# Optimization experiments

Hardware: AMD Instinct MI355X
Metric: run time of the kernel (lower is better)

Reference implementation:

```python
import jax, jax.numpy as jnp
import numpy as np

B, S, NH, HD = 2, 2048, 32, 128     # batch seqs, tokens per seq, heads, head_dim
H = NH * HD                          # hidden = 4096
BLOCK = 64                           # paged KV-cache block size
NBLK = S // BLOCK                    # blocks per sequence
NUM_BLOCKS = B * NBLK                # total cache blocks


def alibi_slopes(n):
    # n is a power of two: slope_i = 2^(-8*(i+1)/n)
    return np.asarray([2.0 ** (-8.0 * (i + 1) / n) for i in range(n)], dtype=np.float32)


def setup_inputs() -> dict:
    key = jax.random.key(0)
    k1, k2, k3 = jax.random.split(key, 3)
    hidden_states = jax.random.normal(k1, (B * S, H), jnp.float32)
    w_pack = jax.random.normal(k2, (H, 3 * H), jnp.float32) * 0.02
    o_proj_w = jax.random.normal(k3, (H, H), jnp.float32) * 0.02
    k_cache = jnp.zeros((NUM_BLOCKS, BLOCK, NH, HD), jnp.float32)
    v_cache = jnp.zeros((NUM_BLOCKS, BLOCK, NH, HD), jnp.float32)
    block_offsets = jnp.arange(NUM_BLOCKS, dtype=jnp.int32).reshape(B, NBLK)
    return {
        "hidden_states": hidden_states,
        "w_pack": w_pack,
        "o_proj_w": o_proj_w,
        "k_cache": k_cache,
        "v_cache": v_cache,
        "block_offsets": block_offsets,
    }


def reference(hidden_states, w_pack, o_proj_w, k_cache, v_cache, block_offsets):
    # fused QKV projection, chunk(3, -1)
    qkv = hidden_states @ w_pack                      # [B*S, 3H]
    q, k, v = jnp.split(qkv, 3, axis=-1)
    q = q.reshape(B, S, NH, HD)
    k = k.reshape(B, NBLK, BLOCK, NH, HD)
    v = v.reshape(B, NBLK, BLOCK, NH, HD)

    # fill_kv_cache: scatter new K/V into paged cache blocks
    k_cache = k_cache.at[block_offsets].set(k)        # [NUM_BLOCKS, BLOCK, NH, HD]
    v_cache = v_cache.at[block_offsets].set(v)

    # paged read: gather non-contiguous blocks back per sequence
    kg = k_cache[block_offsets].reshape(B, S, NH, HD)
    vg = v_cache[block_offsets].reshape(B, S, NH, HD)

    slopes = jnp.asarray(alibi_slopes(NH))            # [NH]
    scale = 1.0 / jnp.sqrt(jnp.float32(HD))
    scores = jnp.einsum('bqhd,bkhd->bhqk', q, kg) * scale   # [B,NH,S,S]
    pos = jnp.arange(S)
    # ALiBi bias: slope * key_position (row-shift invariant under softmax)
    scores = scores + slopes[None, :, None, None] * pos[None, None, None, :]
    causal = pos[:, None] >= pos[None, :]             # [S,S]
    scores = jnp.where(causal[None, None], scores, jnp.float32(-1e30))
    probs = jax.nn.softmax(scores, axis=-1)
    attn = jnp.einsum('bhqk,bkhd->bqhd', probs, vg).reshape(B * S, H)
    return attn @ o_proj_w
```

## Files before the change

kernel.cpp:

```cpp
#include <hip/hip_runtime.h>
#include <hip/hip_bf16.h>
#include <stdint.h>

typedef __attribute__((ext_vector_type(4))) float f32x4;
typedef __attribute__((ext_vector_type(8))) __bf16 bf16x8;
typedef __attribute__((ext_vector_type(8))) unsigned short u16x8;
typedef __attribute__((ext_vector_type(4))) unsigned short u16x4;
typedef __attribute__((ext_vector_type(4))) unsigned int u32x4;

#define GLL16(g, l) __builtin_amdgcn_global_load_lds( \
    (const __attribute__((address_space(1))) unsigned int*)(uintptr_t)(g), \
    (__attribute__((address_space(3))) unsigned int*)(uintptr_t)(l), 16, 0, 0)

__device__ __forceinline__ unsigned short bf16u(float f) {
  return __builtin_bit_cast(unsigned short, __float2bfloat16(f));
}

#define PB 2
#define PS 2048
#define PNH 32
#define PHD 128
#define PH 4096
#define P3H 12288

__global__ __launch_bounds__(256)
void cvt_f32_bf16(const float* __restrict__ in, unsigned short* __restrict__ out, int n) {
  int stride = gridDim.x * blockDim.x;
  for (int i = blockIdx.x * blockDim.x + threadIdx.x; i * 8 < n; i += stride) {
    int base = i * 8;
    f32x4 a = *(const f32x4*)(in + base);
    f32x4 b = *(const f32x4*)(in + base + 4);
    u16x8 o;
#pragma unroll
    for (int j = 0; j < 4; ++j) { o[j] = bf16u(a[j]); o[4 + j] = bf16u(b[j]); }
    *(u16x8*)(out + base) = o;
  }
}

__global__ __launch_bounds__(256)
void transpose_cvt(const float* __restrict__ in, unsigned short* __restrict__ out,
                   int K, int N) {
  __shared__ __align__(16) unsigned short tile[64][68];
  int k0 = blockIdx.y * 64, n0 = blockIdx.x * 64;
  int t = threadIdx.x;
  int rr = t >> 4, cc = (t & 15) * 4;
#pragma unroll
  for (int p = 0; p < 4; ++p) {
    int r = rr + p * 16;
    f32x4 v = *(const f32x4*)(in + (size_t)(k0 + r) * N + n0 + cc);
    u16x4 w;
#pragma unroll
    for (int j = 0; j < 4; ++j) w[j] = bf16u(v[j]);
    *(u16x4*)&tile[r][cc] = w;
  }
  __syncthreads();
#pragma unroll
  for (int p = 0; p < 4; ++p) {
    int nl = rr + p * 16;
    u16x4 w;
#pragma unroll
    for (int j = 0; j < 4; ++j) w[j] = tile[cc + j][nl];
    *(u16x4*)(out + (size_t)(n0 + nl) * K + k0 + cc) = w;
  }
}

#define GLLP(TT, P) do { int sb_ = ((TT) & 3) << 15; \
    const unsigned short* s_ = (P) == 0 ? aSrc0 : (P) == 1 ? aSrc1 : (P) == 2 ? bSrc0 : bSrc1; \
    GLL16(s_ + (size_t)(TT) * 32, smem + sb_ + ((P) << 13) + (wave << 10)); } while (0)

#define RD_AV(DST, BUFP, I) DST[I] = *(const bf16x8*)((BUFP) + (((wm << 7) + ((I) << 4) + lr) << 6) + lchunk)
#define RD_BV(DST, BUFP, J) DST[J] = *(const bf16x8*)((BUFP) + 16384 + (((wn << 6) + ((J) << 4) + lr) << 6) + lchunk)

#define SGB __builtin_amdgcn_sched_group_barrier

#define TILE(TC, AC, AN, DOSTAGE, DOREAD, VM, DOBAR) do { \
    char* nA_ = smem + ((((TC) + 1) & 3) << 15); \
    __builtin_amdgcn_s_setprio(1); \
    _Pragma("unroll") \
    for (int g = 0; g < 4; ++g) { \
      if (DOREAD) { RD_AV(AN, nA_, 2 * g); RD_AV(AN, nA_, 2 * g + 1); } \
      if (DOSTAGE) GLLP((TC) + 3, g); \
      _Pragma("unroll") \
      for (int i = 2 * g; i < 2 * g + 2; ++i) \
        _Pragma("unroll") \
        for (int j = 0; j < 4; ++j) \
          acc[i][j] = __builtin_amdgcn_mfma_f32_16x16x32_bf16(AC[i], bvv[j], acc[i][j], 0, 0, 0); \
      SGB(0x100, 2, 0); SGB(0x020, 1, 0); SGB(0x008, 8, 0); \
    } \
    if (DOREAD) { RD_BV(bvv, nA_, 0); RD_BV(bvv, nA_, 1); RD_BV(bvv, nA_, 2); RD_BV(bvv, nA_, 3); } \
    __builtin_amdgcn_s_setprio(0); \
    if ((VM) == 4)      asm volatile("s_waitcnt vmcnt(4)" ::: "memory"); \
    else if ((VM) == 0) asm volatile("s_waitcnt vmcnt(0)" ::: "memory"); \
    if (DOBAR) __builtin_amdgcn_s_barrier(); \
  } while (0)

template<int OUTF32>
__global__ __launch_bounds__(512, 2)
void gemm256(const unsigned short* __restrict__ A, const unsigned short* __restrict__ Bt,
             void* __restrict__ Cv, int M, int N, int K) {
  __shared__ __align__(16) char smem[131072];
  const int tid = threadIdx.x;
  const int wave = tid >> 6, lane = tid & 63;
  const int lr = lane & 15, lg = lane >> 4;
  const int wm = wave >> 2, wn = wave & 3;
  const int lchunk = (lg ^ ((lr >> 1) & 3)) << 4;
  const int nbn = N >> 8;
  const int nwg = (M >> 8) * nbn;
  int bid = blockIdx.x;
  int qq = nwg >> 3;
  int wg = (bid & 7) * qq + (bid >> 3);
  int bm = wg / nbn, bn = wg % nbn;
  const size_t arow = (size_t)bm << 8;
  const size_t brow = (size_t)bn << 8;

  const int srow = (wave << 4) + (lane >> 2);
  const int scol = ((lane & 3) ^ ((lane >> 3) & 3)) << 3;
  const unsigned short* aSrc0 = A  + (arow + srow) * K + scol;
  const unsigned short* aSrc1 = A  + (arow + 128 + srow) * K + scol;
  const unsigned short* bSrc0 = Bt + (brow + srow) * K + scol;
  const unsigned short* bSrc1 = Bt + (brow + 128 + srow) * K + scol;

  f32x4 acc[8][4] = {};

#pragma unroll
  for (int p = 0; p < 4; ++p) GLLP(0, p);
#pragma unroll
  for (int p = 0; p < 4; ++p) GLLP(1, p);
#pragma unroll
  for (int p = 0; p < 4; ++p) GLLP(2, p);
  asm volatile("s_waitcnt vmcnt(4)" ::: "memory");
  __builtin_amdgcn_s_barrier();

  bf16x8 avA[8], avB[8], bvv[4];
  {
    char* b0 = smem;
#pragma unroll
    for (int i = 0; i < 8; ++i) RD_AV(avA, b0, i);
#pragma unroll
    for (int j = 0; j < 4; ++j) RD_BV(bvv, b0, j);
  }

  for (int p = 0; p < 62; ++p) {
    int t = 2 * p;
    TILE(t,     avA, avB, 1, 1, 4, 1);
    TILE(t + 1, avB, avA, 1, 1, 4, 1);
  }
  TILE(124, avA, avB, 1, 1, 4, 1);
  TILE(125, avB, avA, 0, 1, 0, 1);
  TILE(126, avA, avB, 0, 1, -1, 0);
  TILE(127, avB, avA, 0, 0, -1, 0);

  int crow = (bm << 8) + (wm << 7) + (lg << 2);
  int ccol = (bn << 8) + (wn << 6) + lr;
#pragma unroll
  for (int i = 0; i < 8; ++i)
#pragma unroll
    for (int j = 0; j < 4; ++j)
#pragma unroll
      for (int r = 0; r < 4; ++r) {
        size_t off = (size_t)(crow + (i << 4) + r) * N + ccol + (j << 4);
        if (OUTF32) ((float*)Cv)[off] = acc[i][j][r];
        else        ((unsigned short*)Cv)[off] = bf16u(acc[i][j][r]);
      }
}

__global__ __launch_bounds__(512, 2)
void attn_kernel(const unsigned short* __restrict__ qkv, unsigned short* __restrict__ out) {
  __shared__ __align__(16) unsigned short Ks[2][64 * 128];
  __shared__ __align__(16) unsigned short Vt[128 * 64];
  __shared__ __align__(16) unsigned short Ps[8][32 * 72];
  int tid = threadIdx.x, wave = tid >> 6, lane = tid & 63;
  int lr = lane & 15, lg = lane >> 4;
  int idx = blockIdx.x;
  int qtsel = idx & 7, h = (idx >> 3) & 31, bsel = idx >> 8;
  int qt = bsel ? qtsel : 7 - qtsel;
  size_t rb = (size_t)bsel * PS;
  int qcol = h << 7, kcol = PH + (h << 7), vcol = 2 * PH + (h << 7);
  int q0 = (qt << 8) + (wave << 5);

  bf16x8 aq[2][4];
#pragma unroll
  for (int qs = 0; qs < 2; ++qs)
#pragma unroll
    for (int f = 0; f < 4; ++f)
      aq[qs][f] = *(const bf16x8*)(qkv + (rb + q0 + (qs << 4) + lr) * P3H + qcol + (f << 5) + (lg << 3));

  float m_run[2][4], l_run[2][4];
#pragma unroll
  for (int qs = 0; qs < 2; ++qs)
#pragma unroll
    for (int r = 0; r < 4; ++r) { m_run[qs][r] = -1e30f; l_run[qs][r] = 0.f; }
  f32x4 acc_o[2][8] = {};

  float slope2 = __builtin_amdgcn_exp2f(-(float)(h + 1) * 0.25f) * 1.44269504f;
  const float scale2 = 0.08838834764831845f * 1.44269504f;

  char* KsB = (char*)Ks;
  char* VtB = (char*)Vt;
  const int kk0 = (tid & 31) << 1;
  const int d0 = (tid >> 5) << 3;

  {
    size_t krow = rb;
#pragma unroll
    for (int i = 0; i < 2; ++i) {
      int pf = (wave << 11) | (i << 10) | (lane << 4);
      int row = pf >> 8;
      int lch = ((pf >> 4) & 15) ^ (row & 7);
      GLL16(qkv + (krow + row) * P3H + kcol + (lch << 3), KsB + (wave << 11) + (i << 10));
    }
  }
  u32x4 vr0 = *(const u32x4*)(qkv + (rb + kk0 + 0) * P3H + vcol + d0);
  u32x4 vr1 = *(const u32x4*)(qkv + (rb + kk0 + 1) * P3H + vcol + d0);

  const int tmax = 4 * qt + 3;
  for (int t = 0; t <= tmax; ++t) {
    int cur = t & 1;
    char* KsCur = KsB + (cur << 14);
    char* KsNxt = KsB + ((cur ^ 1) << 14);
    bool more = (t < tmax);

    u32x4 nv0 = {}, nv1 = {};
    if (more) {
      size_t krow = rb + ((size_t)(t + 1) << 6);
#pragma unroll
      for (int i = 0; i < 2; ++i) {
        int pf = (wave << 11) | (i << 10) | (lane << 4);
        int row = pf >> 8;
        int lch = ((pf >> 4) & 15) ^ (row & 7);
        GLL16(qkv + (krow + row) * P3H + kcol + (lch << 3), KsNxt + (wave << 11) + (i << 10));
      }
      nv0 = *(const u32x4*)(qkv + (krow + kk0 + 0) * P3H + vcol + d0);
      nv1 = *(const u32x4*)(qkv + (krow + kk0 + 1) * P3H + vcol + d0);
    }

    if (more) asm volatile("s_waitcnt vmcnt(4)" ::: "memory");
    else      asm volatile("s_waitcnt vmcnt(0)" ::: "memory");

    {
      const unsigned short* e0 = (const unsigned short*)&vr0;
      const unsigned short* e1 = (const unsigned short*)&vr1;
#pragma unroll
      for (int j = 0; j < 8; ++j) {
        int d = d0 + j;
        unsigned int w = (unsigned int)e0[j] | ((unsigned int)e1[j] << 16);
        int byteoff = ((d << 7) + (kk0 << 1)) ^ ((d & 7) << 4);
        *(unsigned int*)(VtB + byteoff) = w;
      }
    }
    asm volatile("s_waitcnt lgkmcnt(0)" ::: "memory");
    __builtin_amdgcn_s_barrier();

    f32x4 sc[2][4];
    __builtin_amdgcn_s_setprio(1);
#pragma unroll
    for (int f = 0; f < 4; ++f) {
      f32x4 c0 = {}, c1 = {};
#pragma unroll
      for (int ks = 0; ks < 4; ++ks) {
        int kkr = (f << 4) + lr;
        int ch = (lg + (ks << 2)) ^ (kkr & 7);
        bf16x8 bk = *(const bf16x8*)(KsCur + (kkr << 8) + (ch << 4));
        c0 = __builtin_amdgcn_mfma_f32_16x16x32_bf16(aq[0][ks], bk, c0, 0, 0, 0);
        c1 = __builtin_amdgcn_mfma_f32_16x16x32_bf16(aq[1][ks], bk, c1, 0, 0, 0);
      }
      sc[0][f] = c0; sc[1][f] = c1;
    }
    __builtin_amdgcn_s_setprio(0);

    int kvb = t << 6;
    bool needmask = (kvb + 63 > q0);
#pragma unroll
    for (int qs = 0; qs < 2; ++qs) {
      float vals[4][4];
#pragma unroll
      for (int f = 0; f < 4; ++f) {
        int kv = kvb + (f << 4) + lr;
        float bias = slope2 * (float)kv;
#pragma unroll
        for (int r = 0; r < 4; ++r) {
          float v = sc[qs][f][r] * scale2 + bias;
          if (needmask && kv > q0 + (qs << 4) + (lg << 2) + r) v = -1e30f;
          vals[r][f] = v;
        }
      }
      float alpha[4];
#pragma unroll
      for (int r = 0; r < 4; ++r) {
        float mr = fmaxf(fmaxf(vals[r][0], vals[r][1]), fmaxf(vals[r][2], vals[r][3]));
#pragma unroll
        for (int d2 = 1; d2 < 16; d2 <<= 1) mr = fmaxf(mr, __shfl_xor(mr, d2, 16));
        float mnew = fmaxf(m_run[qs][r], mr);
        alpha[r] = __builtin_amdgcn_exp2f(m_run[qs][r] - mnew);
        m_run[qs][r] = mnew;
      }
#pragma unroll
      for (int r = 0; r < 4; ++r) {
        float s = 0.f;
#pragma unroll
        for (int f = 0; f < 4; ++f) {
          float p = __builtin_amdgcn_exp2f(vals[r][f] - m_run[qs][r]);
          s += p;
          Ps[wave][((qs << 4) + (lg << 2) + r) * 72 + (f << 4) + lr] = bf16u(p);
        }
        l_run[qs][r] = l_run[qs][r] * alpha[r] + s;
      }
#pragma unroll
      for (int d = 0; d < 8; ++d) {
        f32x4 a4 = acc_o[qs][d];
#pragma unroll
        for (int r = 0; r < 4; ++r) a4[r] *= alpha[r];
        acc_o[qs][d] = a4;
      }
    }

    bf16x8 pa[2][2];
#pragma unroll
    for (int qs = 0; qs < 2; ++qs)
#pragma unroll
      for (int ks = 0; ks < 2; ++ks)
        pa[qs][ks] = *(const bf16x8*)((char*)&Ps[wave][0] + ((qs << 4) + lr) * 144 + (ks << 6) + (lg << 4));
    __builtin_amdgcn_s_setprio(1);
#pragma unroll
    for (int d = 0; d < 8; ++d) {
#pragma unroll
      for (int ks = 0; ks < 2; ++ks) {
        int dr = (d << 4) + lr;
        int ch = (lg + (ks << 2)) ^ (dr & 7);
        bf16x8 bv = *(const bf16x8*)(VtB + (dr << 7) + (ch << 4));
        acc_o[0][d] = __builtin_amdgcn_mfma_f32_16x16x32_bf16(pa[0][ks], bv, acc_o[0][d], 0, 0, 0);
        acc_o[1][d] = __builtin_amdgcn_mfma_f32_16x16x32_bf16(pa[1][ks], bv, acc_o[1][d], 0, 0, 0);
      }
    }
    __builtin_amdgcn_s_setprio(0);
    __builtin_amdgcn_s_barrier();

    if (more) { vr0 = nv0; vr1 = nv1; }
  }

#pragma unroll
  for (int qs = 0; qs < 2; ++qs) {
    float rinv[4];
#pragma unroll
    for (int r = 0; r < 4; ++r) {
      float s = l_run[qs][r];
#pragma unroll
      for (int d2 = 1; d2 < 16; d2 <<= 1) s += __shfl_xor(s, d2, 16);
      rinv[r] = 1.f / s;
    }
#pragma unroll
    for (int d = 0; d < 8; ++d)
#pragma unroll
      for (int r = 0; r < 4; ++r) {
        float o = acc_o[qs][d][r] * rinv[r];
        out[(rb + q0 + (qs << 4) + (lg << 2) + r) * PH + (h << 7) + (d << 4) + lr] = bf16u(o);
      }
  }
}

extern "C" void kernel_launch(void* const* d_in, const int* in_sizes, int n_in,
                              void* d_out, int out_size, void* d_ws, size_t ws_size,
                              hipStream_t stream) {
  const float* hidden = (const float*)d_in[0];
  const float* w_pack = (const float*)d_in[1];
  const float* o_proj = (const float*)d_in[2];

  char* ws = (char*)d_ws;
  unsigned short* wpackT = (unsigned short*)(ws);
  unsigned short* qkv    = (unsigned short*)(ws + 100663296);
  unsigned short* oprojT = (unsigned short*)(ws + 201326592);
  unsigned short* hbf    = (unsigned short*)(ws + 234881024);
  unsigned short* attnb  = hbf;

  int M = PB * PS;

  cvt_f32_bf16<<<2048, 256, 0, stream>>>(hidden, hbf, M * PH);
  transpose_cvt<<<dim3(P3H / 64, PH / 64), 256, 0, stream>>>(w_pack, wpackT, PH, P3H);
  transpose_cvt<<<dim3(PH / 64, PH / 64), 256, 0, stream>>>(o_proj, oprojT, PH, PH);
  gemm256<0><<<(M / 256) * (P3H / 256), 512, 0, stream>>>(hbf, wpackT, qkv, M, P3H, PH);
  attn_kernel<<<PB * PNH * (PS / 256), 512, 0, stream>>>(qkv, attnb);
  gemm256<1><<<(M / 256) * (PH / 256), 512, 0, stream>>>(attnb, oprojT, d_out, M, PH, PH);
}
```

Measured before the change: 744.2 us.

## Split GEMM 256x256 tile across 16 waves with 64x64 per-wave subtiles

Relaunches both projection GEMMs with 1024 threads per block, giving each of 16 waves a 64x64 output subtile instead of 8 waves with 128x64. Each wave now stages one row-slice of A and B per K-step, and reads its LDS fragments at the start of each tile. This drops the register double-buffering of A and the sched_group_barrier interleaving. The aim is to hide memory and LDS latency with more resident waves and fewer accumulator registers per wave. The trade-off is that less LDS-to-MFMA overlap now happens inside each wave, and the tighter launch bound may constrain register allocation.

```diff
diff --git a/kernel.cpp b/kernel.cpp
--- a/kernel.cpp
+++ b/kernel.cpp
@@ -64,38 +64,35 @@
   }
 }
 
-#define GLLP(TT, P) do { int sb_ = ((TT) & 3) << 15; \
-    const unsigned short* s_ = (P) == 0 ? aSrc0 : (P) == 1 ? aSrc1 : (P) == 2 ? bSrc0 : bSrc1; \
-    GLL16(s_ + (size_t)(TT) * 32, smem + sb_ + ((P) << 13) + (wave << 10)); } while (0)
-
-#define RD_AV(DST, BUFP, I) DST[I] = *(const bf16x8*)((BUFP) + (((wm << 7) + ((I) << 4) + lr) << 6) + lchunk)
-#define RD_BV(DST, BUFP, J) DST[J] = *(const bf16x8*)((BUFP) + 16384 + (((wn << 6) + ((J) << 4) + lr) << 6) + lchunk)
-
-#define SGB __builtin_amdgcn_sched_group_barrier
-
-#define TILE(TC, AC, AN, DOSTAGE, DOREAD, VM, DOBAR) do { \
-    char* nA_ = smem + ((((TC) + 1) & 3) << 15); \
+#define STAGE16(TT) do { int sb_ = ((TT) & 3) << 15; \
+    GLL16(aSrc + (size_t)(TT) * 32, smem + sb_ + (wave << 10)); \
+    GLL16(bSrc + (size_t)(TT) * 32, smem + sb_ + 16384 + (wave << 10)); } while (0)
+
+#define TILE16(T, DOSTAGE, VM, DOBAR) do { \
+    char* cb_ = smem + (((T) & 3) << 15); \
+    if (DOSTAGE) STAGE16((T) + 3); \
+    bf16x8 av[4], bv[4]; \
+    _Pragma("unroll") \
+    for (int j = 0; j < 4; ++j) \
+      bv[j] = *(const bf16x8*)(cb_ + 16384 + (((wn << 6) + (j << 4) + lr) << 6) + lchunk); \
+    _Pragma("unroll") \
+    for (int i = 0; i < 4; ++i) \
+      av[i] = *(const bf16x8*)(cb_ + (((wm << 6) + (i << 4) + lr) << 6) + lchunk); \
     __builtin_amdgcn_s_setprio(1); \
     _Pragma("unroll") \
-    for (int g = 0; g < 4; ++g) { \
-      if (DOREAD) { RD_AV(AN, nA_, 2 * g); RD_AV(AN, nA_, 2 * g + 1); } \
-      if (DOSTAGE) GLLP((TC) + 3, g); \
+    for (int i = 0; i < 4; ++i) \
       _Pragma("unroll") \
-      for (int i = 2 * g; i < 2 * g + 2; ++i) \
-        _Pragma("unroll") \
-        for (int j = 0; j < 4; ++j) \
-          acc[i][j] = __builtin_amdgcn_mfma_f32_16x16x32_bf16(AC[i], bvv[j], acc[i][j], 0, 0, 0); \
-      SGB(0x100, 2, 0); SGB(0x020, 1, 0); SGB(0x008, 8, 0); \
-    } \
-    if (DOREAD) { RD_BV(bvv, nA_, 0); RD_BV(bvv, nA_, 1); RD_BV(bvv, nA_, 2); RD_BV(bvv, nA_, 3); } \
+      for (int j = 0; j < 4; ++j) \
+        acc[i][j] = __builtin_amdgcn_mfma_f32_16x16x32_bf16(av[i], bv[j], acc[i][j], 0, 0, 0); \
     __builtin_amdgcn_s_setprio(0); \
     if ((VM) == 4)      asm volatile("s_waitcnt vmcnt(4)" ::: "memory"); \
+    else if ((VM) == 2) asm volatile("s_waitcnt vmcnt(2)" ::: "memory"); \
     else if ((VM) == 0) asm volatile("s_waitcnt vmcnt(0)" ::: "memory"); \
     if (DOBAR) __builtin_amdgcn_s_barrier(); \
   } while (0)
 
 template<int OUTF32>
-__global__ __launch_bounds__(512, 2)
+__global__ __launch_bounds__(1024, 4)
 void gemm256(const unsigned short* __restrict__ A, const unsigned short* __restrict__ Bt,
              void* __restrict__ Cv, int M, int N, int K) {
   __shared__ __align__(16) char smem[131072];
@@ -115,45 +112,24 @@
 
   const int srow = (wave << 4) + (lane >> 2);
   const int scol = ((lane & 3) ^ ((lane >> 3) & 3)) << 3;
-  const unsigned short* aSrc0 = A  + (arow + srow) * K + scol;
-  const unsigned short* aSrc1 = A  + (arow + 128 + srow) * K + scol;
-  const unsigned short* bSrc0 = Bt + (brow + srow) * K + scol;
-  const unsigned short* bSrc1 = Bt + (brow + 128 + srow) * K + scol;
-
-  f32x4 acc[8][4] = {};
-
-#pragma unroll
-  for (int p = 0; p < 4; ++p) GLLP(0, p);
-#pragma unroll
-  for (int p = 0; p < 4; ++p) GLLP(1, p);
-#pragma unroll
-  for (int p = 0; p < 4; ++p) GLLP(2, p);
+  const unsigned short* aSrc = A  + (arow + srow) * K + scol;
+  const unsigned short* bSrc = Bt + (brow + srow) * K + scol;
+
+  f32x4 acc[4][4] = {};
+
+  STAGE16(0); STAGE16(1); STAGE16(2);
   asm volatile("s_waitcnt vmcnt(4)" ::: "memory");
   __builtin_amdgcn_s_barrier();
 
-  bf16x8 avA[8], avB[8], bvv[4];
-  {
-    char* b0 = smem;
-#pragma unroll
-    for (int i = 0; i < 8; ++i) RD_AV(avA, b0, i);
-#pragma unroll
-    for (int j = 0; j < 4; ++j) RD_BV(bvv, b0, j);
-  }
-
-  for (int p = 0; p < 62; ++p) {
-    int t = 2 * p;
-    TILE(t,     avA, avB, 1, 1, 4, 1);
-    TILE(t + 1, avB, avA, 1, 1, 4, 1);
-  }
-  TILE(124, avA, avB, 1, 1, 4, 1);
-  TILE(125, avB, avA, 0, 1, 0, 1);
-  TILE(126, avA, avB, 0, 1, -1, 0);
-  TILE(127, avB, avA, 0, 0, -1, 0);
-
-  int crow = (bm << 8) + (wm << 7) + (lg << 2);
+  for (int t = 0; t < 125; ++t) TILE16(t, 1, 4, 1);
+  TILE16(125, 0, 2, 1);
+  TILE16(126, 0, 0, 1);
+  TILE16(127, 0, -1, 0);
+
+  int crow = (bm << 8) + (wm << 6) + (lg << 2);
   int ccol = (bn << 8) + (wn << 6) + lr;
 #pragma unroll
-  for (int i = 0; i < 8; ++i)
+  for (int i = 0; i < 4; ++i)
 #pragma unroll
     for (int j = 0; j < 4; ++j)
 #pragma unroll
@@ -377,7 +353,7 @@
   cvt_f32_bf16<<<2048, 256, 0, stream>>>(hidden, hbf, M * PH);
   transpose_cvt<<<dim3(P3H / 64, PH / 64), 256, 0, stream>>>(w_pack, wpackT, PH, P3H);
   transpose_cvt<<<dim3(PH / 64, PH / 64), 256, 0, stream>>>(o_proj, oprojT, PH, PH);
-  gemm256<0><<<(M / 256) * (P3H / 256), 512, 0, stream>>>(hbf, wpackT, qkv, M, P3H, PH);
+  gemm256<0><<<(M / 256) * (P3H / 256), 1024, 0, stream>>>(hbf, wpackT, qkv, M, P3H, PH);
   attn_kernel<<<PB * PNH * (PS / 256), 512, 0, stream>>>(qkv, attnb);
-  gemm256<1><<<(M / 256) * (PH / 256), 512, 0, stream>>>(attnb, oprojT, d_out, M, PH, PH);
-}
+  gemm256<1><<<(M / 256) * (PH / 256), 1024, 0, stream>>>(attnb, oprojT, d_out, M, PH, PH);
+}
```

Result: no change. 748.9 us (+0.6%).
